# Performance work log

Hardware: AMD Instinct MI355X
Metric: run time of the kernel (lower is better)

## Reference

```python
import jax, jax.numpy as jnp
import numpy as np

N_NODES = 300000
B = 100000
MEM = 256
NF = 256
MSG = 256


def setup_inputs() -> dict:
    key = jax.random.key(0)
    ks = jax.random.split(key, 10)
    s_msg = 1.0 / np.sqrt(NF + MEM + MSG)
    s_gru = 1.0 / np.sqrt(MEM)
    return {
        "memory": jax.random.normal(ks[0], (N_NODES, MEM), jnp.float32),
        "messages_state": jnp.zeros((N_NODES, MSG), jnp.float32),
        "last_update": jnp.zeros((N_NODES,), jnp.float32),
        "node_idxs": jnp.arange(B, dtype=jnp.int32),
        "node_features": jax.random.normal(ks[1], (B, NF), jnp.float32),
        "edge_features": jax.random.normal(ks[2], (B, MSG), jnp.float32),
        "timestamps": jax.random.uniform(ks[3], (B,), jnp.float32) * 1000.0,
        "W1": jax.random.normal(ks[4], (NF + MEM + MSG, MSG), jnp.float32) * s_msg,
        "b1": jnp.zeros((MSG,), jnp.float32),
        "W2": jax.random.normal(ks[5], (MSG, MSG), jnp.float32) * (1.0 / np.sqrt(MSG)),
        "b2": jnp.zeros((MSG,), jnp.float32),
        "Wih": jax.random.normal(ks[6], (3 * MEM, MSG), jnp.float32) * s_gru,
        "Whh": jax.random.normal(ks[7], (3 * MEM, MEM), jnp.float32) * s_gru,
        "bih": jnp.zeros((3 * MEM,), jnp.float32),
        "bhh": jnp.zeros((3 * MEM,), jnp.float32),
    }


def reference(memory, messages_state, last_update, node_idxs, node_features,
              edge_features, timestamps, W1, b1, W2, b2, Wih, Whh, bih, bhh):
    # Gather per-event node memory: [B, MEM]
    h = memory[node_idxs]
    # message_fn: 2-layer MLP on cat([node_features, node_memory, edge_features])
    x = jnp.concatenate([node_features, h, edge_features], axis=1)  # [B, NF+MEM+MSG]
    m = jnp.maximum(x @ W1 + b1, 0.0) @ W2 + b2  # [B, MSG]
    # GRUCell (torch semantics): gates order r, z, n
    gx = m @ Wih.T + bih   # [B, 3*MEM]
    gh = h @ Whh.T + bhh   # [B, 3*MEM]
    xr, xz, xn = jnp.split(gx, 3, axis=1)
    hr, hz, hn = jnp.split(gh, 3, axis=1)
    r = jax.nn.sigmoid(xr + hr)
    z = jax.nn.sigmoid(xz + hz)
    n = jnp.tanh(xn + r * hn)
    h_new = (1.0 - z) * n + z * h  # [B, MEM]
    # Scatter back into node tables
    memory_new = memory.at[node_idxs].set(h_new)
    messages_new = messages_state.at[node_idxs].set(m)
    last_update_new = last_update.at[node_idxs].set(timestamps)
    return memory_new, messages_new, last_update_new
```

## Files before the change

### kernel.cpp

```cpp
#include <hip/hip_runtime.h>
#include <math.h>

#define MEMD 256
#define BM   32
#define NT   256

__device__ __forceinline__ float sigmoidf(float x) {
    return 1.0f / (1.0f + __expf(-x));
}

__device__ __forceinline__ void col_fma(const float (*A)[MEMD], const float* Wcol, float* acc) {
    for (int k4 = 0; k4 < 64; ++k4) {
        float w0 = Wcol[(4 * k4 + 0) * MEMD];
        float w1 = Wcol[(4 * k4 + 1) * MEMD];
        float w2 = Wcol[(4 * k4 + 2) * MEMD];
        float w3 = Wcol[(4 * k4 + 3) * MEMD];
#pragma unroll
        for (int r = 0; r < BM; ++r) {
            float4 av = ((const float4*)A[r])[k4];
            acc[r] = fmaf(av.x, w0, acc[r]);
            acc[r] = fmaf(av.y, w1, acc[r]);
            acc[r] = fmaf(av.z, w2, acc[r]);
            acc[r] = fmaf(av.w, w3, acc[r]);
        }
    }
}

__device__ __forceinline__ void row_fma(const float (*A)[MEMD], const float* wrow, float* acc) {
    for (int k4 = 0; k4 < 64; ++k4) {
        float4 wv = ((const float4*)wrow)[k4];
#pragma unroll
        for (int r = 0; r < BM; ++r) {
            float4 av = ((const float4*)A[r])[k4];
            acc[r] = fmaf(av.x, wv.x, acc[r]);
            acc[r] = fmaf(av.y, wv.y, acc[r]);
            acc[r] = fmaf(av.z, wv.z, acc[r]);
            acc[r] = fmaf(av.w, wv.w, acc[r]);
        }
    }
}

__global__ __launch_bounds__(NT, 2)
void tgn_fused(const float* __restrict__ memory,
               const int*   __restrict__ node_idxs,
               const float* __restrict__ nf,
               const float* __restrict__ ef,
               const float* __restrict__ tstamps,
               const float* __restrict__ W1, const float* __restrict__ b1,
               const float* __restrict__ W2, const float* __restrict__ b2,
               const float* __restrict__ Wih, const float* __restrict__ Whh,
               const float* __restrict__ bih, const float* __restrict__ bhh,
               float* __restrict__ out_mem, float* __restrict__ out_msg,
               float* __restrict__ out_lu)
{
    __shared__ float hs[BM][MEMD];
    __shared__ float ms[BM][MEMD];
    __shared__ float xs[BM][64];
    __shared__ int   idxs[BM];

    const int t = threadIdx.x;
    const int row0 = blockIdx.x * BM;

    if (t < BM) idxs[t] = node_idxs[row0 + t];
    __syncthreads();

    for (int j = t; j < BM * 64; j += NT) {
        int r = j >> 6, c4 = j & 63;
        ((float4*)hs[r])[c4] = ((const float4*)(memory + (size_t)idxs[r] * MEMD))[c4];
    }
    __syncthreads();

    float acc[BM];
    {
        float b = b1[t];
#pragma unroll
        for (int r = 0; r < BM; ++r) acc[r] = b;
    }

    col_fma(hs, W1 + 256 * MEMD + t, acc);

    for (int seg = 0; seg < 2; ++seg) {
        const float* src = seg ? ef : nf;
        const int kbase = seg ? 512 : 0;
        for (int kb = 0; kb < 256; kb += 64) {
            __syncthreads();
#pragma unroll
            for (int i = 0; i < 2; ++i) {
                int j = i * NT + t;
                int r = j >> 4, c4 = j & 15;
                ((float4*)xs[r])[c4] =
                    ((const float4*)(src + (size_t)(row0 + r) * MEMD))[(kb >> 2) + c4];
            }
            __syncthreads();
            const float* Wcol = W1 + (size_t)(kbase + kb) * MEMD + t;
            for (int k4 = 0; k4 < 16; ++k4) {
                float w0 = Wcol[(4 * k4 + 0) * MEMD];
                float w1 = Wcol[(4 * k4 + 1) * MEMD];
                float w2 = Wcol[(4 * k4 + 2) * MEMD];
                float w3 = Wcol[(4 * k4 + 3) * MEMD];
#pragma unroll
                for (int r = 0; r < BM; ++r) {
                    float4 xv = ((const float4*)xs[r])[k4];
                    acc[r] = fmaf(xv.x, w0, acc[r]);
                    acc[r] = fmaf(xv.y, w1, acc[r]);
                    acc[r] = fmaf(xv.z, w2, acc[r]);
                    acc[r] = fmaf(xv.w, w3, acc[r]);
                }
            }
        }
    }

    __syncthreads();
#pragma unroll
    for (int r = 0; r < BM; ++r) ms[r][t] = fmaxf(acc[r], 0.0f);
    __syncthreads();

    float acc2[BM];
    {
        float b = b2[t];
#pragma unroll
        for (int r = 0; r < BM; ++r) acc2[r] = b;
    }
    col_fma(ms, W2 + t, acc2);

#pragma unroll
    for (int r = 0; r < BM; ++r)
        out_msg[(size_t)idxs[r] * MEMD + t] = acc2[r];
    __syncthreads();
#pragma unroll
    for (int r = 0; r < BM; ++r) ms[r][t] = acc2[r];
    __syncthreads();

    float rv[BM];
    {
        float b = bih[t] + bhh[t];
#pragma unroll
        for (int r = 0; r < BM; ++r) rv[r] = b;
        row_fma(ms, Wih + (size_t)t * MEMD, rv);
        row_fma(hs, Whh + (size_t)t * MEMD, rv);
#pragma unroll
        for (int r = 0; r < BM; ++r) rv[r] = sigmoidf(rv[r]);
    }
    float zv[BM];
    {
        float b = bih[MEMD + t] + bhh[MEMD + t];
#pragma unroll
        for (int r = 0; r < BM; ++r) zv[r] = b;
        row_fma(ms, Wih + (size_t)(MEMD + t) * MEMD, zv);
        row_fma(hs, Whh + (size_t)(MEMD + t) * MEMD, zv);
#pragma unroll
        for (int r = 0; r < BM; ++r) zv[r] = sigmoidf(zv[r]);
    }
    float axn[BM], ahn[BM];
    {
        float bx = bih[2 * MEMD + t];
        float bh = bhh[2 * MEMD + t];
#pragma unroll
        for (int r = 0; r < BM; ++r) { axn[r] = bx; ahn[r] = bh; }
        row_fma(ms, Wih + (size_t)(2 * MEMD + t) * MEMD, axn);
        row_fma(hs, Whh + (size_t)(2 * MEMD + t) * MEMD, ahn);
    }

#pragma unroll
    for (int r = 0; r < BM; ++r) {
        float n = tanhf(axn[r] + rv[r] * ahn[r]);
        float h = hs[r][t];
        float hn = fmaf(zv[r], h - n, n);
        out_mem[(size_t)idxs[r] * MEMD + t] = hn;
    }
    if (t < BM) out_lu[idxs[t]] = tstamps[row0 + t];
}

extern "C" void kernel_launch(void* const* d_in, const int* in_sizes, int n_in,
                              void* d_out, int out_size, void* d_ws, size_t ws_size,
                              hipStream_t stream)
{
    const float* memory      = (const float*)d_in[0];
    const float* messages    = (const float*)d_in[1];
    const float* last_update = (const float*)d_in[2];
    const int*   node_idxs   = (const int*)  d_in[3];
    const float* nf          = (const float*)d_in[4];
    const float* ef          = (const float*)d_in[5];
    const float* tstamps     = (const float*)d_in[6];
    const float* W1          = (const float*)d_in[7];
    const float* b1          = (const float*)d_in[8];
    const float* W2          = (const float*)d_in[9];
    const float* b2          = (const float*)d_in[10];
    const float* Wih         = (const float*)d_in[11];
    const float* Whh         = (const float*)d_in[12];
    const float* bih         = (const float*)d_in[13];
    const float* bhh         = (const float*)d_in[14];

    const int n_nodes = in_sizes[2];
    const int Bn      = in_sizes[3];

    float* out_mem = (float*)d_out;
    float* out_msg = out_mem + (size_t)n_nodes * MEMD;
    float* out_lu  = out_msg + (size_t)n_nodes * MEMD;

    hipMemcpyAsync(out_mem, memory,      (size_t)n_nodes * MEMD * sizeof(float),
                   hipMemcpyDeviceToDevice, stream);
    hipMemcpyAsync(out_msg, messages,    (size_t)n_nodes * MEMD * sizeof(float),
                   hipMemcpyDeviceToDevice, stream);
    hipMemcpyAsync(out_lu,  last_update, (size_t)n_nodes * sizeof(float),
                   hipMemcpyDeviceToDevice, stream);

    dim3 grid(Bn / BM);
    tgn_fused<<<grid, NT, 0, stream>>>(memory, node_idxs, nf, ef, tstamps,
                                       W1, b1, W2, b2, Wih, Whh, bih, bhh,
                                       out_mem, out_msg, out_lu);
}
```

Baseline: 4.049 ms.

## Retile fused TGN kernel to 8x4 register tiles with transposed GRU weights

Restructures the fused message-MLP plus GRU kernel so each thread computes an 8-row by 4-column float4 register tile, reusing each weight load across rows. A small pre-kernel transposes Wih/Whh into a global buffer so gate weights are read contiguously per output column, replacing per-thread row-strided weight reads. Inputs nf/ef/h are now read directly from global rather than staged in shared memory, and occupancy is raised to 3 blocks per SM. This trades shared-memory reuse of activations for fewer, wider weight loads and more FMAs per load, at the cost of repeated global reads of activations and an extra transpose launch.

```diff
diff --git a/kernel.cpp b/kernel.cpp
--- a/kernel.cpp
+++ b/kernel.cpp
@@ -4,43 +4,42 @@
 #define MEMD 256
 #define BM   32
 #define NT   256
-
-__device__ __forceinline__ float sigmoidf(float x) {
-    return 1.0f / (1.0f + __expf(-x));
-}
-
-__device__ __forceinline__ void col_fma(const float (*A)[MEMD], const float* Wcol, float* acc) {
-    for (int k4 = 0; k4 < 64; ++k4) {
-        float w0 = Wcol[(4 * k4 + 0) * MEMD];
-        float w1 = Wcol[(4 * k4 + 1) * MEMD];
-        float w2 = Wcol[(4 * k4 + 2) * MEMD];
-        float w3 = Wcol[(4 * k4 + 3) * MEMD];
-#pragma unroll
-        for (int r = 0; r < BM; ++r) {
-            float4 av = ((const float4*)A[r])[k4];
-            acc[r] = fmaf(av.x, w0, acc[r]);
-            acc[r] = fmaf(av.y, w1, acc[r]);
-            acc[r] = fmaf(av.z, w2, acc[r]);
-            acc[r] = fmaf(av.w, w3, acc[r]);
-        }
-    }
-}
-
-__device__ __forceinline__ void row_fma(const float (*A)[MEMD], const float* wrow, float* acc) {
-    for (int k4 = 0; k4 < 64; ++k4) {
-        float4 wv = ((const float4*)wrow)[k4];
-#pragma unroll
-        for (int r = 0; r < BM; ++r) {
-            float4 av = ((const float4*)A[r])[k4];
-            acc[r] = fmaf(av.x, wv.x, acc[r]);
-            acc[r] = fmaf(av.y, wv.y, acc[r]);
-            acc[r] = fmaf(av.z, wv.z, acc[r]);
-            acc[r] = fmaf(av.w, wv.w, acc[r]);
-        }
-    }
-}
-
-__global__ __launch_bounds__(NT, 2)
+#define RW   8
+
+__device__ float g_WT[2 * 3 * MEMD * MEMD];
+
+__global__ void transpose_gates(const float* __restrict__ Wih,
+                                const float* __restrict__ Whh)
+{
+    __shared__ float tile[32][33];
+    const float* src = blockIdx.z ? Whh : Wih;
+    float* dst = g_WT + (size_t)blockIdx.z * 3 * MEMD * MEMD;
+    const int j0 = blockIdx.x * 32;
+    const int k0 = blockIdx.y * 32;
+    const int tx = threadIdx.x & 31, ty = threadIdx.x >> 5;
+#pragma unroll
+    for (int r = ty; r < 32; r += 8)
+        tile[r][tx] = src[(size_t)(j0 + r) * MEMD + (k0 + tx)];
+    __syncthreads();
+#pragma unroll
+    for (int r = ty; r < 32; r += 8)
+        dst[(size_t)(k0 + r) * (3 * MEMD) + (j0 + tx)] = tile[tx][r];
+}
+
+__device__ __forceinline__ float sigmoidf_(float x) { return 1.0f / (1.0f + __expf(-x)); }
+
+__device__ __forceinline__ void fma4(float4& a, float s, const float4& w) {
+    a.x = fmaf(s, w.x, a.x);
+    a.y = fmaf(s, w.y, a.y);
+    a.z = fmaf(s, w.z, a.z);
+    a.w = fmaf(s, w.w, a.w);
+}
+
+#define FMA16(ACC, A, W) \
+    do { fma4(ACC, (A).x, (W)[0]); fma4(ACC, (A).y, (W)[1]); \
+         fma4(ACC, (A).z, (W)[2]); fma4(ACC, (A).w, (W)[3]); } while (0)
+
+__global__ __launch_bounds__(NT, 3)
 void tgn_fused(const float* __restrict__ memory,
                const int*   __restrict__ node_idxs,
                const float* __restrict__ nf,
@@ -48,127 +47,201 @@
                const float* __restrict__ tstamps,
                const float* __restrict__ W1, const float* __restrict__ b1,
                const float* __restrict__ W2, const float* __restrict__ b2,
-               const float* __restrict__ Wih, const float* __restrict__ Whh,
                const float* __restrict__ bih, const float* __restrict__ bhh,
                float* __restrict__ out_mem, float* __restrict__ out_msg,
                float* __restrict__ out_lu)
 {
-    __shared__ float hs[BM][MEMD];
     __shared__ float ms[BM][MEMD];
-    __shared__ float xs[BM][64];
-    __shared__ int   idxs[BM];
-
-    const int t = threadIdx.x;
+
+    const int t  = threadIdx.x;
+    const int ln = t & 63;
+    const int wv = t >> 6;
+    const int rq = ln >> 4;
+    const int cq = ln & 15;
+    const int wc = wv * 16 + cq;
+    const int c0 = wc * 4;
+    const int rbase = rq * 8;
     const int row0 = blockIdx.x * BM;
 
-    if (t < BM) idxs[t] = node_idxs[row0 + t];
-    __syncthreads();
-
-    for (int j = t; j < BM * 64; j += NT) {
-        int r = j >> 6, c4 = j & 63;
-        ((float4*)hs[r])[c4] = ((const float4*)(memory + (size_t)idxs[r] * MEMD))[c4];
-    }
-    __syncthreads();
-
-    float acc[BM];
-    {
-        float b = b1[t];
-#pragma unroll
-        for (int r = 0; r < BM; ++r) acc[r] = b;
-    }
-
-    col_fma(hs, W1 + 256 * MEMD + t, acc);
-
-    for (int seg = 0; seg < 2; ++seg) {
-        const float* src = seg ? ef : nf;
-        const int kbase = seg ? 512 : 0;
-        for (int kb = 0; kb < 256; kb += 64) {
-            __syncthreads();
-#pragma unroll
-            for (int i = 0; i < 2; ++i) {
-                int j = i * NT + t;
-                int r = j >> 4, c4 = j & 15;
-                ((float4*)xs[r])[c4] =
-                    ((const float4*)(src + (size_t)(row0 + r) * MEMD))[(kb >> 2) + c4];
-            }
-            __syncthreads();
-            const float* Wcol = W1 + (size_t)(kbase + kb) * MEMD + t;
-            for (int k4 = 0; k4 < 16; ++k4) {
-                float w0 = Wcol[(4 * k4 + 0) * MEMD];
-                float w1 = Wcol[(4 * k4 + 1) * MEMD];
-                float w2 = Wcol[(4 * k4 + 2) * MEMD];
-                float w3 = Wcol[(4 * k4 + 3) * MEMD];
-#pragma unroll
-                for (int r = 0; r < BM; ++r) {
-                    float4 xv = ((const float4*)xs[r])[k4];
-                    acc[r] = fmaf(xv.x, w0, acc[r]);
-                    acc[r] = fmaf(xv.y, w1, acc[r]);
-                    acc[r] = fmaf(xv.z, w2, acc[r]);
-                    acc[r] = fmaf(xv.w, w3, acc[r]);
-                }
-            }
-        }
-    }
-
-    __syncthreads();
-#pragma unroll
-    for (int r = 0; r < BM; ++r) ms[r][t] = fmaxf(acc[r], 0.0f);
-    __syncthreads();
-
-    float acc2[BM];
-    {
-        float b = b2[t];
-#pragma unroll
-        for (int r = 0; r < BM; ++r) acc2[r] = b;
-    }
-    col_fma(ms, W2 + t, acc2);
-
-#pragma unroll
-    for (int r = 0; r < BM; ++r)
-        out_msg[(size_t)idxs[r] * MEMD + t] = acc2[r];
-    __syncthreads();
-#pragma unroll
-    for (int r = 0; r < BM; ++r) ms[r][t] = acc2[r];
-    __syncthreads();
-
-    float rv[BM];
-    {
-        float b = bih[t] + bhh[t];
-#pragma unroll
-        for (int r = 0; r < BM; ++r) rv[r] = b;
-        row_fma(ms, Wih + (size_t)t * MEMD, rv);
-        row_fma(hs, Whh + (size_t)t * MEMD, rv);
-#pragma unroll
-        for (int r = 0; r < BM; ++r) rv[r] = sigmoidf(rv[r]);
-    }
-    float zv[BM];
-    {
-        float b = bih[MEMD + t] + bhh[MEMD + t];
-#pragma unroll
-        for (int r = 0; r < BM; ++r) zv[r] = b;
-        row_fma(ms, Wih + (size_t)(MEMD + t) * MEMD, zv);
-        row_fma(hs, Whh + (size_t)(MEMD + t) * MEMD, zv);
-#pragma unroll
-        for (int r = 0; r < BM; ++r) zv[r] = sigmoidf(zv[r]);
-    }
-    float axn[BM], ahn[BM];
-    {
-        float bx = bih[2 * MEMD + t];
-        float bh = bhh[2 * MEMD + t];
-#pragma unroll
-        for (int r = 0; r < BM; ++r) { axn[r] = bx; ahn[r] = bh; }
-        row_fma(ms, Wih + (size_t)(2 * MEMD + t) * MEMD, axn);
-        row_fma(hs, Whh + (size_t)(2 * MEMD + t) * MEMD, ahn);
-    }
-
-#pragma unroll
-    for (int r = 0; r < BM; ++r) {
-        float n = tanhf(axn[r] + rv[r] * ahn[r]);
-        float h = hs[r][t];
-        float hn = fmaf(zv[r], h - n, n);
-        out_mem[(size_t)idxs[r] * MEMD + t] = hn;
-    }
-    if (t < BM) out_lu[idxs[t]] = tstamps[row0 + t];
+    int idxv[RW];
+    const float* hb[RW];
+#pragma unroll
+    for (int i = 0; i < RW; ++i) {
+        idxv[i] = node_idxs[row0 + rbase + i];
+        hb[i]   = memory + (size_t)idxv[i] * MEMD;
+    }
+    const float* nfb = nf + (size_t)(row0 + rbase) * MEMD;
+    const float* efb = ef + (size_t)(row0 + rbase) * MEMD;
+
+    const float4* W1f4 = (const float4*)W1;
+
+    float4 acc[RW];
+    {
+        float4 b = ((const float4*)b1)[wc];
+#pragma unroll
+        for (int i = 0; i < RW; ++i) acc[i] = b;
+    }
+    for (int k4 = 0; k4 < 64; ++k4) {
+        float4 wnf[4], whh[4], wef[4];
+#pragma unroll
+        for (int kk = 0; kk < 4; ++kk) {
+            wnf[kk] = W1f4[(size_t)(      4 * k4 + kk) * 64 + wc];
+            whh[kk] = W1f4[(size_t)(256 + 4 * k4 + kk) * 64 + wc];
+            wef[kk] = W1f4[(size_t)(512 + 4 * k4 + kk) * 64 + wc];
+        }
+#pragma unroll
+        for (int i = 0; i < RW; ++i) {
+            float4 a0 = *(const float4*)(nfb + (size_t)i * MEMD + k4 * 4);
+            float4 a1 = *(const float4*)(hb[i] + k4 * 4);
+            float4 a2 = *(const float4*)(efb + (size_t)i * MEMD + k4 * 4);
+            FMA16(acc[i], a0, wnf);
+            FMA16(acc[i], a1, whh);
+            FMA16(acc[i], a2, wef);
+        }
+    }
+#pragma unroll
+    for (int i = 0; i < RW; ++i) {
+        float4 v = acc[i];
+        v.x = fmaxf(v.x, 0.f); v.y = fmaxf(v.y, 0.f);
+        v.z = fmaxf(v.z, 0.f); v.w = fmaxf(v.w, 0.f);
+        ((float4*)ms[rbase + i])[wc] = v;
+    }
+    __syncthreads();
+
+    const float4* W2f4 = (const float4*)W2;
+    float4 acc2[RW];
+    {
+        float4 b = ((const float4*)b2)[wc];
+#pragma unroll
+        for (int i = 0; i < RW; ++i) acc2[i] = b;
+    }
+    for (int k4 = 0; k4 < 64; ++k4) {
+        float4 w[4];
+#pragma unroll
+        for (int kk = 0; kk < 4; ++kk) w[kk] = W2f4[(size_t)(4 * k4 + kk) * 64 + wc];
+#pragma unroll
+        for (int i = 0; i < RW; ++i) {
+            float4 a = ((const float4*)ms[rbase + i])[k4];
+            FMA16(acc2[i], a, w);
+        }
+    }
+    __syncthreads();
+#pragma unroll
+    for (int i = 0; i < RW; ++i) {
+        *(float4*)(out_msg + (size_t)idxv[i] * MEMD + c0) = acc2[i];
+        ((float4*)ms[rbase + i])[wc] = acc2[i];
+    }
+    __syncthreads();
+
+    const float4* WTih = (const float4*)g_WT;
+    const float4* WThh = (const float4*)(g_WT + 3 * MEMD * MEMD);
+
+    float4 gr[RW];
+    {
+        float4 bi = ((const float4*)bih)[wc];
+        float4 bh = ((const float4*)bhh)[wc];
+        float4 b = make_float4(bi.x + bh.x, bi.y + bh.y, bi.z + bh.z, bi.w + bh.w);
+#pragma unroll
+        for (int i = 0; i < RW; ++i) gr[i] = b;
+    }
+    for (int k4 = 0; k4 < 64; ++k4) {
+        float4 wm[4], wh[4];
+#pragma unroll
+        for (int kk = 0; kk < 4; ++kk) {
+            wm[kk] = WTih[(size_t)(4 * k4 + kk) * 192 + wc];
+            wh[kk] = WThh[(size_t)(4 * k4 + kk) * 192 + wc];
+        }
+#pragma unroll
+        for (int i = 0; i < RW; ++i) {
+            float4 am = ((const float4*)ms[rbase + i])[k4];
+            float4 ah = *(const float4*)(hb[i] + k4 * 4);
+            FMA16(gr[i], am, wm);
+            FMA16(gr[i], ah, wh);
+        }
+    }
+#pragma unroll
+    for (int i = 0; i < RW; ++i) {
+        gr[i].x = sigmoidf_(gr[i].x); gr[i].y = sigmoidf_(gr[i].y);
+        gr[i].z = sigmoidf_(gr[i].z); gr[i].w = sigmoidf_(gr[i].w);
+    }
+
+    float4 gh[RW];
+    {
+        float4 b = ((const float4*)bhh)[128 + wc];
+#pragma unroll
+        for (int i = 0; i < RW; ++i) gh[i] = b;
+    }
+    for (int k4 = 0; k4 < 64; ++k4) {
+        float4 w[4];
+#pragma unroll
+        for (int kk = 0; kk < 4; ++kk) w[kk] = WThh[(size_t)(4 * k4 + kk) * 192 + 128 + wc];
+#pragma unroll
+        for (int i = 0; i < RW; ++i) {
+            float4 ah = *(const float4*)(hb[i] + k4 * 4);
+            FMA16(gh[i], ah, w);
+        }
+    }
+    float4 gn[RW];
+    {
+        float4 b = ((const float4*)bih)[128 + wc];
+#pragma unroll
+        for (int i = 0; i < RW; ++i) gn[i] = b;
+    }
+    for (int k4 = 0; k4 < 64; ++k4) {
+        float4 w[4];
+#pragma unroll
+        for (int kk = 0; kk < 4; ++kk) w[kk] = WTih[(size_t)(4 * k4 + kk) * 192 + 128 + wc];
+#pragma unroll
+        for (int i = 0; i < RW; ++i) {
+            float4 am = ((const float4*)ms[rbase + i])[k4];
+            FMA16(gn[i], am, w);
+        }
+    }
+#pragma unroll
+    for (int i = 0; i < RW; ++i) {
+        gn[i].x = tanhf(gn[i].x + gr[i].x * gh[i].x);
+        gn[i].y = tanhf(gn[i].y + gr[i].y * gh[i].y);
+        gn[i].z = tanhf(gn[i].z + gr[i].z * gh[i].z);
+        gn[i].w = tanhf(gn[i].w + gr[i].w * gh[i].w);
+    }
+
+    float4 gz[RW];
+    {
+        float4 bi = ((const float4*)bih)[64 + wc];
+        float4 bh = ((const float4*)bhh)[64 + wc];
+        float4 b = make_float4(bi.x + bh.x, bi.y + bh.y, bi.z + bh.z, bi.w + bh.w);
+#pragma unroll
+        for (int i = 0; i < RW; ++i) gz[i] = b;
+    }
+    for (int k4 = 0; k4 < 64; ++k4) {
+        float4 wm[4], wh[4];
+#pragma unroll
+        for (int kk = 0; kk < 4; ++kk) {
+            wm[kk] = WTih[(size_t)(4 * k4 + kk) * 192 + 64 + wc];
+            wh[kk] = WThh[(size_t)(4 * k4 + kk) * 192 + 64 + wc];
+        }
+#pragma unroll
+        for (int i = 0; i < RW; ++i) {
+            float4 am = ((const float4*)ms[rbase + i])[k4];
+            float4 ah = *(const float4*)(hb[i] + k4 * 4);
+            FMA16(gz[i], am, wm);
+            FMA16(gz[i], ah, wh);
+        }
+    }
+
+#pragma unroll
+    for (int i = 0; i < RW; ++i) {
+        float z0 = sigmoidf_(gz[i].x), z1 = sigmoidf_(gz[i].y);
+        float z2 = sigmoidf_(gz[i].z), z3 = sigmoidf_(gz[i].w);
+        float4 h4 = *(const float4*)(hb[i] + c0);
+        float4 o;
+        o.x = fmaf(z0, h4.x - gn[i].x, gn[i].x);
+        o.y = fmaf(z1, h4.y - gn[i].y, gn[i].y);
+        o.z = fmaf(z2, h4.z - gn[i].z, gn[i].z);
+        o.w = fmaf(z3, h4.w - gn[i].w, gn[i].w);
+        *(float4*)(out_mem + (size_t)idxv[i] * MEMD + c0) = o;
+    }
+    if (t < BM) out_lu[node_idxs[row0 + t]] = tstamps[row0 + t];
 }
 
 extern "C" void kernel_launch(void* const* d_in, const int* in_sizes, int n_in,
@@ -205,8 +278,10 @@
     hipMemcpyAsync(out_lu,  last_update, (size_t)n_nodes * sizeof(float),
                    hipMemcpyDeviceToDevice, stream);
 
+    transpose_gates<<<dim3(24, 8, 2), NT, 0, stream>>>(Wih, Whh);
+
     dim3 grid(Bn / BM);
     tgn_fused<<<grid, NT, 0, stream>>>(memory, node_idxs, nf, ef, tstamps,
-                                       W1, b1, W2, b2, Wih, Whh, bih, bhh,
+                                       W1, b1, W2, b2, bih, bhh,
                                        out_mem, out_msg, out_lu);
 }
```

After: 4.026 ms. About the same (-0.6%).
